# Kernel tuning notes

Measured on AMD Instinct MI355X. Metric: run time of the kernel, lower is better.

Reference implementation:

```python
import jax, jax.numpy as jnp
import numpy as np

N, K, IN_C, OUT_C = 100000, 128, 128, 128


def setup_inputs() -> dict:
    key = jax.random.key(0)
    k1, k2, k3 = jax.random.split(key, 3)
    x = jax.random.normal(k1, (N, IN_C), dtype=jnp.float32)
    U = jax.random.normal(k2, (N, K), dtype=jnp.float32)
    coeffs = jax.random.normal(k3, (OUT_C, K, IN_C), dtype=jnp.float32)
    return {"x": x, "U": U, "coeffs": coeffs}


def reference(x, U, coeffs):
    # U.T @ x : (K, in_channels)
    spec = jnp.einsum('nk,ni->ki', U, x)
    # coeffs * spec, summed over in_channels : (out_channels, K)
    mixed = jnp.einsum('oki,ki->ok', coeffs, spec)
    # U @ mixed : (out_channels, N)
    out = jnp.einsum('nk,ok->on', U, mixed)
    # softmax over N (dim=-1), then transpose -> (N, out_channels)
    return jax.nn.softmax(out, axis=-1).T
```

## Files before the change

kernel.cpp:

```cpp
#include <hip/hip_runtime.h>
#include <math.h>

#define N_PTS 100000
#define KDIM 128
#define CDIM 128
#define TILE_N 64
#define NB1 ((N_PTS + TILE_N - 1) / TILE_N)

typedef short s16x8 __attribute__((ext_vector_type(8)));
typedef float f32x4 __attribute__((ext_vector_type(4)));

static __device__ __forceinline__ unsigned short f2bf(float f) {
    unsigned int u = __float_as_uint(f);
    unsigned int r = (u + 0x7FFFu + ((u >> 16) & 1u)) >> 16;
    return (unsigned short)r;
}
static __device__ __forceinline__ float bf2f(unsigned short h) {
    return __uint_as_float(((unsigned int)h) << 16);
}

static __device__ __forceinline__ void split_trunc(float v, unsigned short& hi, unsigned short& lo) {
    unsigned int u = __float_as_uint(v);
    unsigned int uh = u & 0xFFFF0000u;
    float lf = v - __uint_as_float(uh);
    hi = (unsigned short)(u >> 16);
    lo = (unsigned short)(__float_as_uint(lf) >> 16);
}

__global__ __launch_bounds__(512, 4) void kA(const float* __restrict__ U,
                                             const float* __restrict__ x,
                                             float* __restrict__ partials,
                                             int chunk) {
    __shared__ unsigned short SB[2][4][4096];
    const int tid = threadIdx.x;
    const int b = blockIdx.x;
    const int n_begin = b * chunk;
    const int n_end = min(N_PTS, n_begin + chunk);
    const int lane = tid & 63;
    const int w = tid >> 6;
    const int mtb = (w & 3) * 2;
    const int ntb = (w >> 2) * 4;
    const int quad = lane >> 4;
    const int nl = lane & 15;

    const int sc = tid & 127;
    const int rq = tid >> 7;
    const int sgran = (sc >> 4) * 64 + rq * 16 + (sc & 15);

    f32x4 acc[2][4];
#pragma unroll
    for (int mi = 0; mi < 2; ++mi)
#pragma unroll
        for (int ni = 0; ni < 4; ++ni) acc[mi][ni] = (f32x4)(0.0f);

    float uvA[8], xvA[8], uvB[8], xvB[8];

    auto loadChunk = [&](int ci, float* uv, float* xv) {
        const int r0 = n_begin + ci * 32 + rq * 8;
#pragma unroll
        for (int jj = 0; jj < 8; ++jj) {
            int gn = r0 + jj;
            bool ok = (gn < n_end);
            uv[jj] = ok ? U[(size_t)gn * 128 + sc] : 0.0f;
            xv[jj] = ok ? x[(size_t)gn * 128 + sc] : 0.0f;
        }
    };

    auto splitWrite = [&](int buf, const float* uv, const float* xv) {
        s16x8 uh, ul, xh, xl;
#pragma unroll
        for (int jj = 0; jj < 8; ++jj) {
            unsigned short h, l;
            split_trunc(uv[jj], h, l);
            uh[jj] = (short)h; ul[jj] = (short)l;
            split_trunc(xv[jj], h, l);
            xh[jj] = (short)h; xl[jj] = (short)l;
        }
        *(s16x8*)&SB[buf][0][sgran * 8] = uh;
        *(s16x8*)&SB[buf][1][sgran * 8] = ul;
        *(s16x8*)&SB[buf][2][sgran * 8] = xh;
        *(s16x8*)&SB[buf][3][sgran * 8] = xl;
    };

    auto compute = [&](int buf) {
        s16x8 ah[2], al[2];
#pragma unroll
        for (int mi = 0; mi < 2; ++mi) {
            const int off = ((mtb + mi) * 64 + lane) * 8;
            ah[mi] = *(s16x8*)&SB[buf][0][off];
            al[mi] = *(s16x8*)&SB[buf][1][off];
        }
#pragma unroll
        for (int ni = 0; ni < 4; ++ni) {
            const int off = ((ntb + ni) * 64 + lane) * 8;
            s16x8 bh = *(s16x8*)&SB[buf][2][off];
            s16x8 bl = *(s16x8*)&SB[buf][3][off];
#pragma unroll
            for (int mi = 0; mi < 2; ++mi) {
                acc[mi][ni] = __builtin_amdgcn_mfma_f32_16x16x32_bf16(ah[mi], bh, acc[mi][ni], 0, 0, 0);
                acc[mi][ni] = __builtin_amdgcn_mfma_f32_16x16x32_bf16(al[mi], bh, acc[mi][ni], 0, 0, 0);
                acc[mi][ni] = __builtin_amdgcn_mfma_f32_16x16x32_bf16(ah[mi], bl, acc[mi][ni], 0, 0, 0);
            }
        }
    };

    loadChunk(0, uvA, xvA);
    splitWrite(0, uvA, xvA);
    loadChunk(1, uvB, xvB);
    __syncthreads();

    const int nTrips = chunk >> 6;
    for (int t = 0; t < nTrips; ++t) {
        loadChunk(2 * t + 2, uvA, xvA);
        compute(0);
        splitWrite(1, uvB, xvB);
        __syncthreads();
        loadChunk(2 * t + 3, uvB, xvB);
        compute(1);
        if (t + 1 < nTrips) splitWrite(0, uvA, xvA);
        __syncthreads();
    }

    float* p = partials + (size_t)b * 16384;
#pragma unroll
    for (int mi = 0; mi < 2; ++mi) {
#pragma unroll
        for (int reg = 0; reg < 4; ++reg) {
            int k = (mtb + mi) * 16 + quad * 4 + reg;
#pragma unroll
            for (int ni = 0; ni < 4; ++ni) {
                int i = (ntb + ni) * 16 + nl;
                p[k * 128 + i] = acc[mi][ni][reg];
            }
        }
    }
}

__global__ __launch_bounds__(256) void kA2a(const float* __restrict__ partials,
                                            float* __restrict__ partial2, int nA) {
    const int jc = blockIdx.x >> 3;
    const int s = blockIdx.x & 7;
    const int j = jc * 256 + threadIdx.x;
    const int per = (nA + 7) >> 3;
    int b = s * per;
    const int be = min(b + per, nA);
    float a0 = 0.0f, a1 = 0.0f, a2 = 0.0f, a3 = 0.0f;
    for (; b + 4 <= be; b += 4) {
        a0 += partials[(size_t)(b + 0) * 16384 + j];
        a1 += partials[(size_t)(b + 1) * 16384 + j];
        a2 += partials[(size_t)(b + 2) * 16384 + j];
        a3 += partials[(size_t)(b + 3) * 16384 + j];
    }
    for (; b < be; ++b) a0 += partials[(size_t)b * 16384 + j];
    partial2[(size_t)s * 16384 + j] = (a0 + a1) + (a2 + a3);
}

__global__ __launch_bounds__(256) void kB(const float* __restrict__ coeffs,
                                          const float* __restrict__ partial2,
                                          unsigned short* __restrict__ afrag_hi,
                                          unsigned short* __restrict__ afrag_lo) {
    int wave = (blockIdx.x * 256 + threadIdx.x) >> 6;
    int lane = threadIdx.x & 63;
    int o = wave >> 7;
    int k = wave & 127;
    const int j = k * 128 + lane * 2;
    float2 p0 = *(const float2*)&partial2[j];
    float2 p1 = *(const float2*)&partial2[16384 + j];
    float2 p2 = *(const float2*)&partial2[2 * 16384 + j];
    float2 p3 = *(const float2*)&partial2[3 * 16384 + j];
    float2 p4 = *(const float2*)&partial2[4 * 16384 + j];
    float2 p5 = *(const float2*)&partial2[5 * 16384 + j];
    float2 p6 = *(const float2*)&partial2[6 * 16384 + j];
    float2 p7 = *(const float2*)&partial2[7 * 16384 + j];
    float sx = ((p0.x + p1.x) + (p2.x + p3.x)) + ((p4.x + p5.x) + (p6.x + p7.x));
    float sy = ((p0.y + p1.y) + (p2.y + p3.y)) + ((p4.y + p5.y) + (p6.y + p7.y));
    float2 c2 = *(const float2*)&coeffs[((size_t)o * 128 + k) * 128 + lane * 2];
    float v = c2.x * sx + c2.y * sy;
#pragma unroll
    for (int s = 32; s >= 1; s >>= 1) v += __shfl_xor(v, s);
    if (lane == 0) {
        unsigned short hi = f2bf(v);
        unsigned short lo = f2bf(v - bf2f(hi));
        int idx = ((o >> 4) * 4 + (k >> 5)) * 512 + (((k >> 3) & 3) * 16 + (o & 15)) * 8 + (k & 7);
        afrag_hi[idx] = hi;
        afrag_lo[idx] = lo;
    }
}

__global__ __launch_bounds__(512) void kC1(const float* __restrict__ U,
                                           const unsigned short* __restrict__ afrag_hi,
                                           const unsigned short* __restrict__ afrag_lo,
                                           float* __restrict__ out,
                                           float* __restrict__ m_part,
                                           float* __restrict__ l_part) {
    __shared__ unsigned short Bh[8192];
    __shared__ unsigned short Bl[8192];
    const int tid = threadIdx.x;
    const int b = blockIdx.x;
    const int n0 = b * TILE_N;
    const int lane = tid & 63;
    const int w = tid >> 6;
    const int quad = lane >> 4;
    const int nl = lane & 15;

    {
        const int sn = tid & 63;
        const int k8b = tid >> 6;
        const int gn = n0 + sn;
#pragma unroll
        for (int r = 0; r < 2; ++r) {
            const int k0 = (k8b + r * 8) * 8;
            float4 f0 = make_float4(0, 0, 0, 0), f1 = make_float4(0, 0, 0, 0);
            if (gn < N_PTS) {
                f0 = *(const float4*)&U[(size_t)gn * 128 + k0];
                f1 = *(const float4*)&U[(size_t)gn * 128 + k0 + 4];
            }
            float vv[8] = {f0.x, f0.y, f0.z, f0.w, f1.x, f1.y, f1.z, f1.w};
            s16x8 hh, ll;
#pragma unroll
            for (int jj = 0; jj < 8; ++jj) {
                unsigned short h, l;
                split_trunc(vv[jj], h, l);
                hh[jj] = (short)h;
                ll[jj] = (short)l;
            }
            const int T = (k0 >> 5) * 4 + (sn >> 4);
            const int g = T * 64 + ((k0 >> 3) & 3) * 16 + ((sn & 15) ^ (T & 3));
            *(s16x8*)&Bh[g * 8] = hh;
            *(s16x8*)&Bl[g * 8] = ll;
        }
    }

    s16x8 Ah[4], Al[4];
#pragma unroll
    for (int kc = 0; kc < 4; ++kc) {
        size_t aoff = (size_t)(w * 4 + kc) * 512 + lane * 8;
        Ah[kc] = *(const s16x8*)(afrag_hi + aoff);
        Al[kc] = *(const s16x8*)(afrag_lo + aoff);
    }

    __syncthreads();

    f32x4 acc[4];
#pragma unroll
    for (int nt = 0; nt < 4; ++nt) acc[nt] = (f32x4)(0.0f);

#pragma unroll
    for (int kc = 0; kc < 4; ++kc) {
#pragma unroll
        for (int nt = 0; nt < 4; ++nt) {
            const int T = kc * 4 + nt;
            const int g = T * 64 + quad * 16 + (nl ^ (T & 3));
            s16x8 bh = *(s16x8*)&Bh[g * 8];
            s16x8 bl = *(s16x8*)&Bl[g * 8];
            acc[nt] = __builtin_amdgcn_mfma_f32_16x16x32_bf16(Ah[kc], bh, acc[nt], 0, 0, 0);
            acc[nt] = __builtin_amdgcn_mfma_f32_16x16x32_bf16(Al[kc], bh, acc[nt], 0, 0, 0);
            acc[nt] = __builtin_amdgcn_mfma_f32_16x16x32_bf16(Ah[kc], bl, acc[nt], 0, 0, 0);
        }
    }

#pragma unroll
    for (int nt = 0; nt < 4; ++nt) {
        if (n0 + nt * 16 + nl >= N_PTS) {
#pragma unroll
            for (int reg = 0; reg < 4; ++reg) acc[nt][reg] = -3.4e38f;
        }
    }

    float mb[4];
#pragma unroll
    for (int reg = 0; reg < 4; ++reg)
        mb[reg] = fmaxf(fmaxf(acc[0][reg], acc[1][reg]), fmaxf(acc[2][reg], acc[3][reg]));
#pragma unroll
    for (int s = 1; s < 16; s <<= 1) {
#pragma unroll
        for (int reg = 0; reg < 4; ++reg) mb[reg] = fmaxf(mb[reg], __shfl_xor(mb[reg], s));
    }

#pragma unroll
    for (int nt = 0; nt < 4; ++nt) {
#pragma unroll
        for (int reg = 0; reg < 4; ++reg) acc[nt][reg] = __expf(acc[nt][reg] - mb[reg]);
        int gn = n0 + nt * 16 + nl;
        if (gn < N_PTS)
            *(f32x4*)&out[(size_t)gn * 128 + w * 16 + quad * 4] = acc[nt];
    }

    float ls[4];
#pragma unroll
    for (int reg = 0; reg < 4; ++reg)
        ls[reg] = ((acc[0][reg] + acc[1][reg]) + (acc[2][reg] + acc[3][reg]));
#pragma unroll
    for (int s = 1; s < 16; s <<= 1) {
#pragma unroll
        for (int reg = 0; reg < 4; ++reg) ls[reg] += __shfl_xor(ls[reg], s);
    }

    if (nl == 0) {
#pragma unroll
        for (int reg = 0; reg < 4; ++reg) {
            int o = w * 16 + quad * 4 + reg;
            m_part[(size_t)o * NB1 + b] = mb[reg];
            l_part[(size_t)o * NB1 + b] = ls[reg];
        }
    }
}

__global__ __launch_bounds__(256) void kC2(const float* __restrict__ m_part,
                                           const float* __restrict__ l_part,
                                           float* __restrict__ scale) {
    const int o = blockIdx.x;
    const int tid = threadIdx.x;
    const float* __restrict__ mp = m_part + (size_t)o * NB1;
    const float* __restrict__ lp = l_part + (size_t)o * NB1;
    __shared__ float sm[256];
    float m = -3.4e38f;
    for (int b = tid; b < NB1; b += 256) m = fmaxf(m, mp[b]);
    sm[tid] = m;
    __syncthreads();
    for (int s = 128; s >= 1; s >>= 1) {
        if (tid < s) sm[tid] = fmaxf(sm[tid], sm[tid + s]);
        __syncthreads();
    }
    m = sm[0];
    __syncthreads();
    float l = 0.0f;
    for (int b = tid; b < NB1; b += 256)
        l += lp[b] * __expf(mp[b] - m);
    sm[tid] = l;
    __syncthreads();
    for (int s = 128; s >= 1; s >>= 1) {
        if (tid < s) sm[tid] += sm[tid + s];
        __syncthreads();
    }
    l = sm[0];
    float inv = 1.0f / l;
    for (int b = tid; b < NB1; b += 256)
        scale[(size_t)o * NB1 + b] = __expf(mp[b] - m) * inv;
}

__global__ __launch_bounds__(256) void kC3(float* __restrict__ out,
                                           const float* __restrict__ scale) {
    const int b = blockIdx.x;
    const int tid = threadIdx.x;
    __shared__ float sc[128];
    if (tid < 128) sc[tid] = scale[(size_t)tid * NB1 + b];
    __syncthreads();
    const int n0 = b * TILE_N;
#pragma unroll
    for (int r = 0; r < 8; ++r) {
        int idx = (r * 256 + tid) * 4;
        int n = idx >> 7;
        int o = idx & 127;
        int gn = n0 + n;
        if (gn < N_PTS) {
            float4 v = *(float4*)&out[(size_t)gn * 128 + o];
            v.x *= sc[o];
            v.y *= sc[o + 1];
            v.z *= sc[o + 2];
            v.w *= sc[o + 3];
            *(float4*)&out[(size_t)gn * 128 + o] = v;
        }
    }
}

extern "C" void kernel_launch(void* const* d_in, const int* in_sizes, int n_in,
                              void* d_out, int out_size, void* d_ws, size_t ws_size,
                              hipStream_t stream) {
    const float* x = (const float*)d_in[0];
    const float* U = (const float*)d_in[1];
    const float* coeffs = (const float*)d_in[2];
    float* out = (float*)d_out;

    float* f = (float*)d_ws;
    float* spec = f;
    unsigned short* afrag_hi = (unsigned short*)(f + 16384);
    unsigned short* afrag_lo = (unsigned short*)(f + 16384 + 8192);
    float* m_part = f + 16384 + 16384;
    float* l_part = m_part + (size_t)128 * NB1;
    float* scale = l_part + (size_t)128 * NB1;
    float* partial2 = scale + (size_t)128 * NB1;
    float* partialsA = partial2 + 8 * 16384;
    (void)spec;

    size_t fixed_bytes = ((size_t)(16384 * 2) + (size_t)NB1 * 128 * 3 + (size_t)8 * 16384) * 4;
    int nA = 512;
    if (ws_size > fixed_bytes) {
        size_t avail = (ws_size - fixed_bytes) / 65536;
        if ((size_t)nA > avail) nA = (int)avail;
    } else {
        nA = 1;
    }
    if (nA < 1) nA = 1;
    int chunk = (((N_PTS + nA - 1) / nA) + 63) & ~63;
    int nB = (N_PTS + chunk - 1) / chunk;

    kA<<<nB, 512, 0, stream>>>(U, x, partialsA, chunk);
    kA2a<<<512, 256, 0, stream>>>(partialsA, partial2, nB);
    kB<<<4096, 256, 0, stream>>>(coeffs, partial2, afrag_hi, afrag_lo);
    kC1<<<NB1, 512, 0, stream>>>(U, afrag_hi, afrag_lo, out, m_part, l_part);
    kC2<<<128, 256, 0, stream>>>(m_part, l_part, scale);
    kC3<<<NB1, 256, 0, stream>>>(out, scale);
}
```

Before: 206.8 us.

## Load kA MFMA fragments directly from global memory, dropping LDS staging

The U^T·x reduction kernel no longer stages split bf16 hi/lo tiles in shared memory with double buffering and barriers. Each wave now loads its own fragment rows straight from global memory and does the hi/lo split in registers before the MFMAs. The N chunk alignment drops from 64 to 32 rows to match the new 32-row step. This removes LDS traffic, barriers and the occupancy hint. In exchange, each row is read and split redundantly by several waves, and the per-lane loads are strided, so the kernel leans on the caches.

```diff
diff --git a/kernel.cpp b/kernel.cpp
--- a/kernel.cpp
+++ b/kernel.cpp
@@ -27,11 +27,10 @@
     lo = (unsigned short)(__float_as_uint(lf) >> 16);
 }
 
-__global__ __launch_bounds__(512, 4) void kA(const float* __restrict__ U,
-                                             const float* __restrict__ x,
-                                             float* __restrict__ partials,
-                                             int chunk) {
-    __shared__ unsigned short SB[2][4][4096];
+__global__ __launch_bounds__(512) void kA(const float* __restrict__ U,
+                                          const float* __restrict__ x,
+                                          float* __restrict__ partials,
+                                          int chunk) {
     const int tid = threadIdx.x;
     const int b = blockIdx.x;
     const int n_begin = b * chunk;
@@ -43,82 +42,54 @@
     const int quad = lane >> 4;
     const int nl = lane & 15;
 
-    const int sc = tid & 127;
-    const int rq = tid >> 7;
-    const int sgran = (sc >> 4) * 64 + rq * 16 + (sc & 15);
-
     f32x4 acc[2][4];
 #pragma unroll
     for (int mi = 0; mi < 2; ++mi)
 #pragma unroll
         for (int ni = 0; ni < 4; ++ni) acc[mi][ni] = (f32x4)(0.0f);
 
-    float uvA[8], xvA[8], uvB[8], xvB[8];
-
-    auto loadChunk = [&](int ci, float* uv, float* xv) {
-        const int r0 = n_begin + ci * 32 + rq * 8;
-#pragma unroll
-        for (int jj = 0; jj < 8; ++jj) {
-            int gn = r0 + jj;
-            bool ok = (gn < n_end);
-            uv[jj] = ok ? U[(size_t)gn * 128 + sc] : 0.0f;
-            xv[jj] = ok ? x[(size_t)gn * 128 + sc] : 0.0f;
-        }
-    };
-
-    auto splitWrite = [&](int buf, const float* uv, const float* xv) {
-        s16x8 uh, ul, xh, xl;
-#pragma unroll
-        for (int jj = 0; jj < 8; ++jj) {
-            unsigned short h, l;
-            split_trunc(uv[jj], h, l);
-            uh[jj] = (short)h; ul[jj] = (short)l;
-            split_trunc(xv[jj], h, l);
-            xh[jj] = (short)h; xl[jj] = (short)l;
-        }
-        *(s16x8*)&SB[buf][0][sgran * 8] = uh;
-        *(s16x8*)&SB[buf][1][sgran * 8] = ul;
-        *(s16x8*)&SB[buf][2][sgran * 8] = xh;
-        *(s16x8*)&SB[buf][3][sgran * 8] = xl;
-    };
-
-    auto compute = [&](int buf) {
+    for (int r0 = n_begin; r0 < n_end; r0 += 32) {
+        const int rb = r0 + 8 * quad;
         s16x8 ah[2], al[2];
-#pragma unroll
-        for (int mi = 0; mi < 2; ++mi) {
-            const int off = ((mtb + mi) * 64 + lane) * 8;
-            ah[mi] = *(s16x8*)&SB[buf][0][off];
-            al[mi] = *(s16x8*)&SB[buf][1][off];
-        }
-#pragma unroll
-        for (int ni = 0; ni < 4; ++ni) {
-            const int off = ((ntb + ni) * 64 + lane) * 8;
-            s16x8 bh = *(s16x8*)&SB[buf][2][off];
-            s16x8 bl = *(s16x8*)&SB[buf][3][off];
+        {
+            const float* ubase = U + (size_t)rb * 128 + mtb * 16 + nl;
 #pragma unroll
             for (int mi = 0; mi < 2; ++mi) {
-                acc[mi][ni] = __builtin_amdgcn_mfma_f32_16x16x32_bf16(ah[mi], bh, acc[mi][ni], 0, 0, 0);
-                acc[mi][ni] = __builtin_amdgcn_mfma_f32_16x16x32_bf16(al[mi], bh, acc[mi][ni], 0, 0, 0);
-                acc[mi][ni] = __builtin_amdgcn_mfma_f32_16x16x32_bf16(ah[mi], bl, acc[mi][ni], 0, 0, 0);
-            }
-        }
-    };
-
-    loadChunk(0, uvA, xvA);
-    splitWrite(0, uvA, xvA);
-    loadChunk(1, uvB, xvB);
-    __syncthreads();
-
-    const int nTrips = chunk >> 6;
-    for (int t = 0; t < nTrips; ++t) {
-        loadChunk(2 * t + 2, uvA, xvA);
-        compute(0);
-        splitWrite(1, uvB, xvB);
-        __syncthreads();
-        loadChunk(2 * t + 3, uvB, xvB);
-        compute(1);
-        if (t + 1 < nTrips) splitWrite(0, uvA, xvA);
-        __syncthreads();
+                float v[8];
+#pragma unroll
+                for (int j = 0; j < 8; ++j) v[j] = ubase[(size_t)j * 128 + mi * 16];
+                s16x8 hh, ll;
+#pragma unroll
+                for (int j = 0; j < 8; ++j) {
+                    unsigned short h, l;
+                    split_trunc(v[j], h, l);
+                    hh[j] = (short)h; ll[j] = (short)l;
+                }
+                ah[mi] = hh; al[mi] = ll;
+            }
+        }
+        {
+            const float* xbase = x + (size_t)rb * 128 + ntb * 16 + nl;
+#pragma unroll
+            for (int ni = 0; ni < 4; ++ni) {
+                float v[8];
+#pragma unroll
+                for (int j = 0; j < 8; ++j) v[j] = xbase[(size_t)j * 128 + ni * 16];
+                s16x8 bh, bl;
+#pragma unroll
+                for (int j = 0; j < 8; ++j) {
+                    unsigned short h, l;
+                    split_trunc(v[j], h, l);
+                    bh[j] = (short)h; bl[j] = (short)l;
+                }
+#pragma unroll
+                for (int mi = 0; mi < 2; ++mi) {
+                    acc[mi][ni] = __builtin_amdgcn_mfma_f32_16x16x32_bf16(ah[mi], bh, acc[mi][ni], 0, 0, 0);
+                    acc[mi][ni] = __builtin_amdgcn_mfma_f32_16x16x32_bf16(al[mi], bh, acc[mi][ni], 0, 0, 0);
+                    acc[mi][ni] = __builtin_amdgcn_mfma_f32_16x16x32_bf16(ah[mi], bl, acc[mi][ni], 0, 0, 0);
+                }
+            }
+        }
     }
 
     float* p = partials + (size_t)b * 16384;
@@ -392,7 +363,7 @@
         nA = 1;
     }
     if (nA < 1) nA = 1;
-    int chunk = (((N_PTS + nA - 1) / nA) + 63) & ~63;
+    int chunk = (((N_PTS + nA - 1) / nA) + 31) & ~31;
     int nB = (N_PTS + chunk - 1) / chunk;
 
     kA<<<nB, 512, 0, stream>>>(U, x, partialsA, chunk);
```

Measured after the change: 214.2 us. +3.6%, slower.
